# Kernel optimization log

Measured on AMD Instinct MI355X. Metric: run time of the kernel, lower is better.

Reference implementation:

```python
import jax, jax.numpy as jnp
import numpy as np

N_SIN = 3  # fcn_n_sin (static)


def setup_inputs() -> dict:
    key = jax.random.key(0)
    ks = jax.random.split(key, 5)
    B, I, O, H = 256, 128, 128, 32
    F = 1 + 2 * N_SIN
    return {
        "x": jax.random.normal(ks[0], (B, I), dtype=jnp.float32),
        "W1": jax.random.normal(ks[1], (I, O, H, F), dtype=jnp.float32) * 0.3,
        "W2": jax.random.normal(ks[2], (I, O, 1, H), dtype=jnp.float32) * 0.3,
        "B1": jax.random.normal(ks[3], (I, O, H), dtype=jnp.float32) * 0.1,
        "B2": jax.random.normal(ks[4], (I, O, 1), dtype=jnp.float32) * 0.1,
    }


def reference(x, W1, W2, B1, B2):
    # x: [B, I]; per-(i,o) edge MLP on a scalar input, summed over i.
    omega = (2.0 ** jnp.arange(N_SIN)).astype(x.dtype)          # [S]
    ox = x[..., None] * omega                                    # [B, I, S]
    feat = jnp.concatenate([x[..., None], jnp.sin(ox), jnp.cos(ox)], axis=-1)  # [B, I, 1+2S]
    # First linear: per-edge [F -> H]
    h = jnp.einsum('bif,iohf->bioh', feat, W1) + B1              # [B, I, O, H]
    h = jax.nn.silu(h)
    # Second linear: per-edge [H -> 1], then sum over input dims i
    out = jnp.einsum('bioh,ioh->bio', h, W2[:, :, 0, :]) + B2[:, :, 0]  # [B, I, O]
    return out.sum(axis=1)                                       # [B, O]
```

## Files before the change

### kernel.cpp

```cpp
#include <hip/hip_runtime.h>
#include <hip/hip_bf16.h>

#define B_DIM 256
#define I_DIM 128
#define O_DIM 128
#define H_DIM 32
#define F_DIM 7
#define ICHUNK 8
#define NCHUNK (I_DIM / ICHUNK)

typedef __attribute__((ext_vector_type(8))) short short8;
typedef __attribute__((ext_vector_type(4))) float float4v;

__device__ inline short bf16s(float v) {
    union { __hip_bfloat16 h; short s; } u;
    u.h = __float2bfloat16(v);
    return u.s;
}

__global__ __launch_bounds__(256, 4)
void fcnkan_mfma(const float* __restrict__ x,
                 const float* __restrict__ W1,
                 const float* __restrict__ W2,
                 const float* __restrict__ B1,
                 const float* __restrict__ B2,
                 float* __restrict__ out) {
    const int tid  = threadIdx.x;
    const int o    = blockIdx.x;
    const int ic0  = blockIdx.y * ICHUNK;
    const int w    = tid >> 6;
    const int lane = tid & 63;
    const int m    = lane & 15;
    const int q    = lane >> 4;

    const short8 zero8 = {};

    float b2c = 0.f;
    for (int il = 0; il < ICHUNK; ++il) b2c += B2[(size_t)(ic0 + il) * O_DIM + o];

    float acc[16];
    #pragma unroll
    for (int r = 0; r < 16; ++r) acc[r] = 0.f;

    #pragma unroll 1
    for (int il = 0; il < ICHUNK; ++il) {
        const int i = ic0 + il;

        short8 afrag[4];
        #pragma unroll
        for (int t = 0; t < 4; ++t) {
            float xv = x[(size_t)(w * 64 + t * 16 + m) * I_DIM + i];
            float s1 = __sinf(xv), c1 = __cosf(xv);
            float s2 = 2.f * s1 * c1, c2 = 1.f - 2.f * s1 * s1;
            float s4 = 2.f * s2 * c2, c4 = 1.f - 2.f * s2 * s2;
            short8 a;
            a[0] = bf16s(xv); a[1] = bf16s(s1); a[2] = bf16s(s2); a[3] = bf16s(s4);
            a[4] = bf16s(c1); a[5] = bf16s(c2); a[6] = bf16s(c4); a[7] = 0;
            afrag[t] = (q == 0) ? a : zero8;
        }

        const size_t iobase = (size_t)i * O_DIM + o;
        const size_t w1base = iobase * (H_DIM * F_DIM);
        short8 bfrag[2];
        float  b1v[2], w2v[2];
        #pragma unroll
        for (int nt = 0; nt < 2; ++nt) {
            int h = nt * 16 + m;
            const float* wr = W1 + w1base + (size_t)h * F_DIM;
            short8 bfr;
            #pragma unroll
            for (int f = 0; f < F_DIM; ++f) bfr[f] = bf16s(wr[f]);
            bfr[7] = 0;
            bfrag[nt] = (q == 0) ? bfr : zero8;
            b1v[nt] = B1[iobase * H_DIM + h];
            w2v[nt] = W2[iobase * H_DIM + h];
        }

        #pragma unroll
        for (int nt = 0; nt < 2; ++nt) {
            float4v c0 = {b1v[nt], b1v[nt], b1v[nt], b1v[nt]};
            #pragma unroll
            for (int t = 0; t < 4; ++t) {
                float4v z = __builtin_amdgcn_mfma_f32_16x16x32_bf16(
                    afrag[t], bfrag[nt], c0, 0, 0, 0);
                #pragma unroll
                for (int r = 0; r < 4; ++r) {
                    float zz = z[r];
                    float sg = __builtin_amdgcn_rcpf(1.f + __expf(-zz));
                    acc[t * 4 + r] = fmaf(zz * sg, w2v[nt], acc[t * 4 + r]);
                }
            }
        }
    }

    #pragma unroll
    for (int r = 0; r < 16; ++r) {
        float v = acc[r];
        v += __shfl_xor(v, 1, 64);
        v += __shfl_xor(v, 2, 64);
        v += __shfl_xor(v, 4, 64);
        v += __shfl_xor(v, 8, 64);
        acc[r] = v;
    }

    if (m == 0) {
        #pragma unroll
        for (int t = 0; t < 4; ++t) {
            #pragma unroll
            for (int r = 0; r < 4; ++r) {
                int b = w * 64 + t * 16 + q * 4 + r;
                atomicAdd(&out[(size_t)b * O_DIM + o], acc[t * 4 + r] + b2c);
            }
        }
    }
}

extern "C" void kernel_launch(void* const* d_in, const int* in_sizes, int n_in,
                              void* d_out, int out_size, void* d_ws, size_t ws_size,
                              hipStream_t stream) {
    const float* x  = (const float*)d_in[0];
    const float* W1 = (const float*)d_in[1];
    const float* W2 = (const float*)d_in[2];
    const float* B1 = (const float*)d_in[3];
    const float* B2 = (const float*)d_in[4];
    float* out = (float*)d_out;

    hipMemsetAsync(out, 0, (size_t)out_size * sizeof(float), stream);
    dim3 grid(O_DIM, NCHUNK);
    fcnkan_mfma<<<grid, 256, 0, stream>>>(x, W1, W2, B1, B2, out);
}
```

Before: 122.9 us.

## Stage features and edge weights in shared memory once per block

Precomputes the sin/cos feature vectors for all batch rows and the chunk's input dims once per block into LDS, and cooperatively converts W1/B1/W2 for the chunk into LDS. The inner loop then reads MFMA fragments from shared memory instead of recomputing transcendentals per lane group and re-reading weights in every wave. This adds about 38KB of LDS per block and a barrier, and lowers the occupancy hint, which may reduce latency hiding.

```diff
diff --git a/kernel.cpp b/kernel.cpp
--- a/kernel.cpp
+++ b/kernel.cpp
@@ -18,13 +18,18 @@
     return u.s;
 }
 
-__global__ __launch_bounds__(256, 4)
+__global__ __launch_bounds__(256, 2)
 void fcnkan_mfma(const float* __restrict__ x,
                  const float* __restrict__ W1,
                  const float* __restrict__ W2,
                  const float* __restrict__ B1,
                  const float* __restrict__ B2,
                  float* __restrict__ out) {
+    __shared__ __align__(16) short feat_s[ICHUNK * B_DIM * 8];
+    __shared__ __align__(16) short w1_s[ICHUNK * H_DIM * 8];
+    __shared__ float b1_s[ICHUNK * H_DIM];
+    __shared__ float w2_s[ICHUNK * H_DIM];
+
     const int tid  = threadIdx.x;
     const int o    = blockIdx.x;
     const int ic0  = blockIdx.y * ICHUNK;
@@ -35,8 +40,35 @@
 
     const short8 zero8 = {};
 
-    float b2c = 0.f;
-    for (int il = 0; il < ICHUNK; ++il) b2c += B2[(size_t)(ic0 + il) * O_DIM + o];
+    {
+        const float4* xp = reinterpret_cast<const float4*>(x + (size_t)tid * I_DIM + ic0);
+        float4 x0 = xp[0], x1 = xp[1];
+        float xr[8] = {x0.x, x0.y, x0.z, x0.w, x1.x, x1.y, x1.z, x1.w};
+        #pragma unroll
+        for (int il = 0; il < ICHUNK; ++il) {
+            float xv = xr[il];
+            float s1 = __sinf(xv), c1 = __cosf(xv);
+            float s2 = 2.f * s1 * c1, c2 = 1.f - 2.f * s1 * s1;
+            float s4 = 2.f * s2 * c2, c4 = 1.f - 2.f * s2 * s2;
+            short8 a;
+            a[0] = bf16s(xv); a[1] = bf16s(s1); a[2] = bf16s(s2); a[3] = bf16s(s4);
+            a[4] = bf16s(c1); a[5] = bf16s(c2); a[6] = bf16s(c4); a[7] = 0;
+            *reinterpret_cast<short8*>(feat_s + (il * B_DIM + tid) * 8) = a;
+        }
+    }
+    {
+        int il = tid >> 5, h = tid & 31;
+        size_t iobase = (size_t)(ic0 + il) * O_DIM + o;
+        const float* wr = W1 + iobase * (H_DIM * F_DIM) + h * F_DIM;
+        short8 bfr;
+        #pragma unroll
+        for (int f = 0; f < F_DIM; ++f) bfr[f] = bf16s(wr[f]);
+        bfr[7] = 0;
+        *reinterpret_cast<short8*>(w1_s + tid * 8) = bfr;
+        b1_s[tid] = B1[iobase * H_DIM + h];
+        w2_s[tid] = W2[iobase * H_DIM + h];
+    }
+    __syncthreads();
 
     float acc[16];
     #pragma unroll
@@ -44,36 +76,23 @@
 
     #pragma unroll 1
     for (int il = 0; il < ICHUNK; ++il) {
-        const int i = ic0 + il;
+        const short8* fS = reinterpret_cast<const short8*>(feat_s) + il * B_DIM;
+        const short8* wS = reinterpret_cast<const short8*>(w1_s) + il * H_DIM;
 
         short8 afrag[4];
         #pragma unroll
-        for (int t = 0; t < 4; ++t) {
-            float xv = x[(size_t)(w * 64 + t * 16 + m) * I_DIM + i];
-            float s1 = __sinf(xv), c1 = __cosf(xv);
-            float s2 = 2.f * s1 * c1, c2 = 1.f - 2.f * s1 * s1;
-            float s4 = 2.f * s2 * c2, c4 = 1.f - 2.f * s2 * s2;
-            short8 a;
-            a[0] = bf16s(xv); a[1] = bf16s(s1); a[2] = bf16s(s2); a[3] = bf16s(s4);
-            a[4] = bf16s(c1); a[5] = bf16s(c2); a[6] = bf16s(c4); a[7] = 0;
-            afrag[t] = (q == 0) ? a : zero8;
-        }
+        for (int t = 0; t < 4; ++t)
+            afrag[t] = fS[w * 64 + t * 16 + m];
 
-        const size_t iobase = (size_t)i * O_DIM + o;
-        const size_t w1base = iobase * (H_DIM * F_DIM);
         short8 bfrag[2];
         float  b1v[2], w2v[2];
         #pragma unroll
         for (int nt = 0; nt < 2; ++nt) {
             int h = nt * 16 + m;
-            const float* wr = W1 + w1base + (size_t)h * F_DIM;
-            short8 bfr;
-            #pragma unroll
-            for (int f = 0; f < F_DIM; ++f) bfr[f] = bf16s(wr[f]);
-            bfr[7] = 0;
-            bfrag[nt] = (q == 0) ? bfr : zero8;
-            b1v[nt] = B1[iobase * H_DIM + h];
-            w2v[nt] = W2[iobase * H_DIM + h];
+            short8 b = wS[h];
+            bfrag[nt] = (q == 0) ? b : zero8;
+            b1v[nt] = b1_s[il * H_DIM + h];
+            w2v[nt] = w2_s[il * H_DIM + h];
         }
 
         #pragma unroll
@@ -103,6 +122,9 @@
         acc[r] = v;
     }
 
+    float b2c = 0.f;
+    for (int il = 0; il < ICHUNK; ++il) b2c += B2[(size_t)(ic0 + il) * O_DIM + o];
+
     if (m == 0) {
         #pragma unroll
         for (int t = 0; t < 4; ++t) {
```

New measurement: 107.4 us. 1.14x faster.
